# Kernel optimization log

Hardware: AMD Instinct MI355X
Metric: run time of the kernel (lower is better)

The kernel has to match this reference:

```python
import jax, jax.numpy as jnp
import numpy as np

# Deterministic stand-ins for the torch RNG draws in the original forward
# (rot sampled from {0,40,...,320}, shifts from [-20,20], flips from {2,3}).
ROT_DEG = 40.0          # rotations[1]
SHIFTS = (5, -7)        # roll shifts on (H, W)
FLIP_DIMS = (2, 3)      # flip W and D dims (torch.arange(2,4) both selected)


def _rotate_nn_maps(H, W, deg):
    """Nearest-neighbor inverse-rotation index maps for an HxW grid
    (matches torchvision rotate: nearest interp, expand=False, fill=0)."""
    theta = jnp.deg2rad(jnp.float32(deg))
    cy = (H - 1) / 2.0
    cx = (W - 1) / 2.0
    i = jnp.arange(H, dtype=jnp.float32)[:, None] - cy  # [H,1]
    j = jnp.arange(W, dtype=jnp.float32)[None, :] - cx  # [1,W]
    c, s = jnp.cos(theta), jnp.sin(theta)
    # inverse rotation: map each output pixel back to its source location
    src_i = c * i + s * j + cy
    src_j = -s * i + c * j + cx
    si = jnp.round(src_i).astype(jnp.int32)
    sj = jnp.round(src_j).astype(jnp.int32)
    valid = (si >= 0) & (si < H) & (sj >= 0) & (sj < W)
    return jnp.clip(si, 0, H - 1), jnp.clip(sj, 0, W - 1), valid


def setup_inputs() -> dict:
    key = jax.random.key(0)
    features = jax.random.normal(key, (16, 128, 128, 8, 16), dtype=jnp.float32)
    return {"features": features}


def reference(features):
    # features: [B, H, W, D, F]; one fused gather rotates the (H, W) plane for
    # every (sample, depth, feature) simultaneously, replacing the original
    # per-(sample, feature) Python rotate() loop.
    B, H, W, D, F = features.shape
    si, sj, valid = _rotate_nn_maps(H, W, ROT_DEG)
    rotated = jnp.where(valid[None, :, :, None, None],
                        features[:, si, sj, :, :], 0.0)  # [B,H,W,D,F]
    rolled = jnp.roll(rotated, SHIFTS, axis=(1, 2))
    flipped = jnp.flip(rolled, axis=FLIP_DIMS)
    return flipped
```

## Files before the change

### kernel.cpp

```cpp
#include <hip/hip_runtime.h>
#include <math.h>

#define BB 16
#define HH 128
#define WW 128
#define DD 8
#define FF 16


__global__ __launch_bounds__(256) void aug_kernel(const float4* __restrict__ in,
                                                  float4* __restrict__ out,
                                                  int n_vec4) {
    int tid = blockIdx.x * blockDim.x + threadIdx.x;
    if (tid >= n_vec4) return;

    int t  = tid;
    int f4 = t & 3;   t >>= 2;
    int d  = t & 7;   t >>= 3;
    int w  = t & 127; t >>= 7;
    int h  = t & 127; t >>= 7;
    int b  = t;

    int i = (h + 123) & 127;
    int j = (134 - w) & 127;

    const double c = 0.76604444311897803;
    const double s = 0.64278760968653933;
    const double cy = 63.5, cx = 63.5;
    double di = (double)i - cy;
    double dj = (double)j - cx;
    double src_i = c * di + s * dj + cy;
    double src_j = -s * di + c * dj + cx;
    int si = (int)rint(src_i);
    int sj = (int)rint(src_j);
    bool valid = (si >= 0) & (si < HH) & (sj >= 0) & (sj < WW);

    float4 v = make_float4(0.f, 0.f, 0.f, 0.f);
    if (valid) {
        int dd = 7 - d;
        long long src = ((((long long)b * HH + si) * WW + sj) * DD + dd) * 4 + f4;
        v = in[src];
    }
    out[tid] = v;
}

extern "C" void kernel_launch(void* const* d_in, const int* in_sizes, int n_in,
                              void* d_out, int out_size, void* d_ws, size_t ws_size,
                              hipStream_t stream) {
    const float4* in = (const float4*)d_in[0];
    float4* out = (float4*)d_out;
    int n_vec4 = out_size / 4;
    int block = 256;
    int grid = (n_vec4 + block - 1) / block;
    aug_kernel<<<grid, block, 0, stream>>>(in, out, n_vec4);
}
```

Baseline: 221.8 us.

## Tile output into 32x32 HW blocks with per-thread row loop and nontemporal stores

Replaces the one-thread-per-float4 grid with 256 blocks of 1024 threads. Each block covers a 32x32 spatial tile of one batch, and each thread loops over 32 rows, hoisting the column-dependent rotation terms out of the loop. Output writes use nontemporal stores so they do not pollute the cache. The intent is to cut index arithmetic and improve gather locality. The cost is only 256 blocks, so occupancy and latency hiding may drop.

```diff
diff --git a/kernel.cpp b/kernel.cpp
--- a/kernel.cpp
+++ b/kernel.cpp
@@ -1,56 +1,59 @@
 #include <hip/hip_runtime.h>
 #include <math.h>
 
-#define BB 16
+
+typedef float f32x4 __attribute__((ext_vector_type(4)));
+
 #define HH 128
 #define WW 128
-#define DD 8
-#define FF 16
 
+__global__ __launch_bounds__(1024) void aug_tiled(const f32x4* __restrict__ in,
+                                                  f32x4* __restrict__ out) {
+    int blk = blockIdx.x;
+    int tw0 = (blk & 3) << 5;
+    int th0 = ((blk >> 2) & 3) << 5;
+    int b   = blk >> 4;
 
-__global__ __launch_bounds__(256) void aug_kernel(const float4* __restrict__ in,
-                                                  float4* __restrict__ out,
-                                                  int n_vec4) {
-    int tid = blockIdx.x * blockDim.x + threadIdx.x;
-    if (tid >= n_vec4) return;
+    int t  = threadIdx.x;
+    int f4 = t & 3;
+    int d  = (t >> 2) & 7;
+    int wp = t >> 5;
+    int dd = 7 - d;
 
-    int t  = tid;
-    int f4 = t & 3;   t >>= 2;
-    int d  = t & 7;   t >>= 3;
-    int w  = t & 127; t >>= 7;
-    int h  = t & 127; t >>= 7;
-    int b  = t;
-
-    int i = (h + 123) & 127;
+    int w = tw0 + wp;
     int j = (134 - w) & 127;
 
     const double c = 0.76604444311897803;
     const double s = 0.64278760968653933;
-    const double cy = 63.5, cx = 63.5;
-    double di = (double)i - cy;
-    double dj = (double)j - cx;
-    double src_i = c * di + s * dj + cy;
-    double src_j = -s * di + c * dj + cx;
-    int si = (int)rint(src_i);
-    int sj = (int)rint(src_j);
-    bool valid = (si >= 0) & (si < HH) & (sj >= 0) & (sj < WW);
+    double dj = (double)j - 63.5;
+    double sjc = c * dj + 63.5;
+    double sic = s * dj + 63.5;
 
-    float4 v = make_float4(0.f, 0.f, 0.f, 0.f);
-    if (valid) {
-        int dd = 7 - d;
-        long long src = ((((long long)b * HH + si) * WW + sj) * DD + dd) * 4 + f4;
-        v = in[src];
+    long long base_b = (long long)b * (HH * WW * 8 * 4);
+
+    #pragma unroll 4
+    for (int hp = 0; hp < 32; ++hp) {
+        int h = th0 + hp;
+        int i = (h + 123) & 127;
+        double di = (double)i - 63.5;
+        int si = (int)rint(c * di + sic);
+        int sj = (int)rint(-s * di + sjc);
+        bool valid = (si >= 0) & (si < HH) & (sj >= 0) & (sj < WW);
+
+        f32x4 v = (f32x4)(0.f);
+        if (valid) {
+            long long src = base_b + (long long)(((si * WW + sj) * 8 + dd) * 4 + f4);
+            v = in[src];
+        }
+        long long dst = base_b + (long long)(((h * WW + w) * 8 + d) * 4 + f4);
+        __builtin_nontemporal_store(v, &out[dst]);
     }
-    out[tid] = v;
 }
 
 extern "C" void kernel_launch(void* const* d_in, const int* in_sizes, int n_in,
                               void* d_out, int out_size, void* d_ws, size_t ws_size,
                               hipStream_t stream) {
-    const float4* in = (const float4*)d_in[0];
-    float4* out = (float4*)d_out;
-    int n_vec4 = out_size / 4;
-    int block = 256;
-    int grid = (n_vec4 + block - 1) / block;
-    aug_kernel<<<grid, block, 0, stream>>>(in, out, n_vec4);
+    const f32x4* in = (const f32x4*)d_in[0];
+    f32x4* out = (f32x4*)d_out;
+    aug_tiled<<<256, 1024, 0, stream>>>(in, out);
 }
```

New measurement: 230.5 us. 3.9% more time.
